# Kernel tuning notes

Measured on AMD Instinct MI355X. Metric: run time of the kernel, lower is better.

Reference implementation:

```python
import jax, jax.numpy as jnp
import numpy as np

N_EMBED = 768
NUM_EXPERTS = 8
TOP_K = 2
B, S = 2, 2048
THRESH = 1e-09


def setup_inputs() -> dict:
    key = jax.random.key(0)
    ks = jax.random.split(key, 12)
    d, e, f = N_EMBED, NUM_EXPERTS, 4 * N_EMBED
    s_in = 1.0 / np.sqrt(d)
    s_hid = 1.0 / np.sqrt(f)
    return {
        'x': jax.random.normal(ks[0], (B, S, d), jnp.float32),
        'noise': jax.random.normal(ks[1], (B * S, e), jnp.float32),
        'Wg': jax.random.normal(ks[2], (d, e), jnp.float32) * s_in,
        'bg': jnp.zeros((e,), jnp.float32),
        'Wn': jax.random.normal(ks[3], (d, e), jnp.float32) * s_in,
        'bn': jnp.zeros((e,), jnp.float32),
        'W1': jax.random.normal(ks[4], (e, d, f), jnp.float32) * s_in,
        'b1': jnp.zeros((e, f), jnp.float32),
        'W2': jax.random.normal(ks[5], (e, f, d), jnp.float32) * s_hid,
        'b2': jnp.zeros((e, d), jnp.float32),
    }


def reference(x, noise, Wg, bg, Wn, bn, W1, b1, W2, b2):
    Bsz, Ssz, d = x.shape
    T = Bsz * Ssz
    xr = x.reshape(T, d)  # [T, d]

    # Noisy top-k router
    logits = xr @ Wg + bg                     # [T, E]
    noise_logits = xr @ Wn + bn               # [T, E]
    noisy = logits + noise * jax.nn.softplus(noise_logits)
    vals, idx = jax.lax.top_k(noisy, TOP_K)   # [T, K]
    rows = jnp.arange(T)[:, None]
    sparse = jnp.full_like(noisy, -jnp.inf).at[rows, idx].set(vals)
    probs = jax.nn.softmax(sparse, axis=-1)   # [T, E]; zeros off top-k

    # Gate = prob masked by activation threshold (matches torch dispatch)
    gate = jnp.where(probs > THRESH, probs, 0.0)  # [T, E]

    # Dense per-expert MLP (dropout=0 -> identity), combined by gate
    h = jax.nn.relu(jnp.einsum('td,edf->etf', xr, W1) + b1[:, None, :])  # [E, T, 4d]
    y = jnp.einsum('etf,efd->etd', h, W2) + b2[:, None, :]               # [E, T, d]
    out = jnp.einsum('te,etd->td', gate, y)                              # [T, d]
    return out.reshape(Bsz, Ssz, d)
```

## Files before the change

kernel.cpp:

```cpp
#include <hip/hip_runtime.h>
#include <math.h>

typedef unsigned short u16;
typedef unsigned int u32;

#define D_EMB 768
#define F_HID 3072
#define N_TOK 4096
#define N_PAIR 8192
#define GATE_TH 1e-9f

typedef float f32x4 __attribute__((ext_vector_type(4)));
typedef __bf16 bfrag __attribute__((ext_vector_type(8)));

__device__ inline float b2f(u16 u) {
    union { float f; u32 i; } c; c.i = ((u32)u) << 16; return c.f;
}
__device__ inline u16 f2b(float f) {
    union { float f; u32 i; } c; c.f = f;
    u32 r = c.i + 0x7FFFu + ((c.i >> 16) & 1u);
    return (u16)(r >> 16);
}
__device__ inline f32x4 mfma16(bfrag a, bfrag b, f32x4 c) {
    return __builtin_amdgcn_mfma_f32_16x16x32_bf16(a, b, c, 0, 0, 0);
}
__device__ inline void gll16(const u16* g, u16* l) {
    __builtin_amdgcn_global_load_lds(
        (const __attribute__((address_space(1))) u32*)g,
        (__attribute__((address_space(3))) u32*)l, 16, 0, 0);
}
__device__ inline void sbar() {
    asm volatile("" ::: "memory");
    __builtin_amdgcn_s_barrier();
    asm volatile("" ::: "memory");
}
__device__ inline void waitv0() { asm volatile("s_waitcnt vmcnt(0)" ::: "memory"); }
__device__ inline void waitv4() { asm volatile("s_waitcnt vmcnt(4)" ::: "memory"); }

__global__ void moe_init_kernel(int* __restrict__ cnt) {
    if (threadIdx.x < 8) cnt[threadIdx.x] = 0;
}
__global__ __launch_bounds__(256) void moe_zero_kernel(uint4* __restrict__ out) {
    int i = blockIdx.x * 256 + threadIdx.x;
    out[i] = make_uint4(0, 0, 0, 0);
}

__global__ __launch_bounds__(64) void moe_router_v3(
    const float* __restrict__ x, const float* __restrict__ noise,
    const float* __restrict__ Wg, const float* __restrict__ bg,
    const float* __restrict__ Wn, const float* __restrict__ bn,
    int* __restrict__ tk_e, float* __restrict__ tk_g, int* __restrict__ cnt,
    ushort4* __restrict__ xb4)
{
    const int lane = threadIdx.x;
    const int tl = lane & 7, q = lane >> 3;
    const int t = blockIdx.x * 8 + tl;
    float ag[8] = {}, an[8] = {};
    const float4* xp = (const float4*)(x + (size_t)t * D_EMB + q * 96);
#pragma unroll 4
    for (int k4 = 0; k4 < 24; k4++) {
        float4 xv = xp[k4];
        const int kb = q * 96 + k4 * 4;
#pragma unroll
        for (int c = 0; c < 4; c++) {
            float xc = (&xv.x)[c];
            const float4* wg = (const float4*)(Wg + (size_t)(kb + c) * 8);
            const float4* wn = (const float4*)(Wn + (size_t)(kb + c) * 8);
            float4 g0 = wg[0], g1 = wg[1], n0 = wn[0], n1 = wn[1];
            ag[0] += xc * g0.x; ag[1] += xc * g0.y; ag[2] += xc * g0.z; ag[3] += xc * g0.w;
            ag[4] += xc * g1.x; ag[5] += xc * g1.y; ag[6] += xc * g1.z; ag[7] += xc * g1.w;
            an[0] += xc * n0.x; an[1] += xc * n0.y; an[2] += xc * n0.z; an[3] += xc * n0.w;
            an[4] += xc * n1.x; an[5] += xc * n1.y; an[6] += xc * n1.z; an[7] += xc * n1.w;
        }
    }
#pragma unroll
    for (int e = 0; e < 8; e++) {
        ag[e] += __shfl_xor(ag[e], 8);  an[e] += __shfl_xor(an[e], 8);
        ag[e] += __shfl_xor(ag[e], 16); an[e] += __shfl_xor(an[e], 16);
        ag[e] += __shfl_xor(ag[e], 32); an[e] += __shfl_xor(an[e], 32);
    }
    if (q == 0) {
        float best = -INFINITY, sec = -INFINITY; int be = 0, se = 0;
#pragma unroll
        for (int e = 0; e < 8; e++) {
            float nl = an[e] + bn[e];
            float sp = nl > 0.f ? nl + log1pf(expf(-nl)) : log1pf(expf(nl));
            float v = ag[e] + bg[e] + noise[(size_t)t * 8 + e] * sp;
            if (v > best) { sec = best; se = be; best = v; be = e; }
            else if (v > sec) { sec = v; se = e; }
        }
        float ex = expf(sec - best);
        float g1 = 1.f / (1.f + ex), g2 = ex / (1.f + ex);
        tk_e[t * 2 + 0] = (g1 > GATE_TH) ? be : -1; tk_g[t * 2 + 0] = g1;
        tk_e[t * 2 + 1] = (g2 > GATE_TH) ? se : -1; tk_g[t * 2 + 1] = g2;
        if (g1 > GATE_TH) atomicAdd(&cnt[be], 1);
        if (g2 > GATE_TH) atomicAdd(&cnt[se], 1);
    }
    if (xb4) {
        const int t0 = blockIdx.x * 8;
        for (int i = lane; i < 8 * 192; i += 64) {
            int ti = i / 192, c = i - ti * 192;
            float4 v = *(const float4*)(x + (size_t)(t0 + ti) * D_EMB + c * 4);
            ushort4 o;
            o.x = f2b(v.x); o.y = f2b(v.y); o.z = f2b(v.z); o.w = f2b(v.w);
            xb4[(size_t)(t0 + ti) * 192 + c] = o;
        }
    }
}

__global__ void moe_offsets_kernel(const int* __restrict__ cnt,
                                   int* __restrict__ off, int* __restrict__ cursor) {
    if (threadIdx.x == 0) {
        int s = 0;
        for (int e = 0; e < 8; e++) { off[e] = s; cursor[e] = s; s += cnt[e]; }
    }
}
__global__ void moe_scatter_kernel(const int* __restrict__ tk_e, const float* __restrict__ tk_g,
                                   int* __restrict__ cursor, int* __restrict__ plist,
                                   float* __restrict__ pg, int* __restrict__ pos) {
    int i = blockIdx.x * 256 + threadIdx.x;
    if (i < N_PAIR) {
        int e = tk_e[i];
        if (e >= 0) {
            int p = atomicAdd(&cursor[e], 1);
            plist[p] = i >> 1;
            pg[p] = tk_g[i];
            pos[i] = p;
        }
    }
}

__global__ __launch_bounds__(256) void moe_transcvt_kernel(
    const float* __restrict__ in, u16* __restrict__ out, int R, int C) {
    __shared__ float tile[32][33];
    const int z = blockIdx.z;
    const int c0 = blockIdx.x * 32, r0 = blockIdx.y * 32;
    const int tx = threadIdx.x & 31, ty = threadIdx.x >> 5;
    const size_t base = (size_t)z * R * C;
#pragma unroll
    for (int j = 0; j < 32; j += 8)
        tile[ty + j][tx] = in[base + (size_t)(r0 + ty + j) * C + c0 + tx];
    __syncthreads();
#pragma unroll
    for (int j = 0; j < 32; j += 8)
        out[base + (size_t)(c0 + ty + j) * R + r0 + tx] = f2b(tile[tx][ty + j]);
}

__global__ __launch_bounds__(256) void moe_ffn1_kernel(
    const u16* __restrict__ xb, const u16* __restrict__ wt, const float* __restrict__ b1,
    const int* __restrict__ plist, const int* __restrict__ cnt, const int* __restrict__ off,
    u16* __restrict__ h, int P0, int P1)
{
    __shared__ __align__(16) u16 As[2][128 * 32];
    __shared__ __align__(16) u16 Bs[2][128 * 32];
    const int GX = 24, GY = 16;
    int f = blockIdx.x + GX * (blockIdx.y + GY * blockIdx.z);
    int swz = (f & 7) * 384 + (f >> 3);
    int nb = swz % GX;
    int t2 = swz / GX;
    int mb = t2 % GY;
    int e  = t2 / GY;

    int lo = off[e], hi = lo + cnt[e];
    if (lo < P0) lo = P0;
    if (hi > P1) hi = P1;
    const int Cl = hi - lo;
    if (Cl <= 0) return;
    const int n0 = nb * 128;
    const int tid = threadIdx.x;
    const int lane = tid & 63, wave = tid >> 6;
    const int wr = wave >> 1, wc = wave & 1;
    const int qq = lane >> 4, r = lane & 15;
    const int sig = (r & 3) ^ ((r >> 2) & 3);
    const int sa = ((qq ^ sig) << 3);
    const int srow = tid >> 2;
    const int gq = (tid & 3) ^ ((tid >> 2) & 3) ^ ((tid >> 4) & 3);

    const u16* bsrc[2];
#pragma unroll
    for (int j = 0; j < 2; j++)
        bsrc[j] = wt + ((size_t)e * F_HID + n0 + j * 64 + srow) * D_EMB + gq * 8;

    for (int m0 = mb * 128; m0 < Cl; m0 += GY * 128) {
        const u16* asrc[2];
#pragma unroll
        for (int j = 0; j < 2; j++) {
            int mr = m0 + j * 64 + srow;
            if (mr > Cl - 1) mr = Cl - 1;
            asrc[j] = xb + (size_t)plist[lo + mr] * D_EMB + gq * 8;
        }
        f32x4 acc[4][4] = {};

        auto stage = [&](int kt, int buf) {
            const int k0 = kt * 32;
#pragma unroll
            for (int j = 0; j < 2; j++)
                gll16(asrc[j] + k0, &As[buf][j * 2048 + wave * 512]);
#pragma unroll
            for (int j = 0; j < 2; j++)
                gll16(bsrc[j] + k0, &Bs[buf][j * 2048 + wave * 512]);
        };
        auto compute = [&](int buf) {
            bfrag af[4], bf[4];
#pragma unroll
            for (int i = 0; i < 4; i++) {
                af[i] = *(const bfrag*)(&As[buf][(wr * 64 + i * 16 + r) * 32 + sa]);
                bf[i] = *(const bfrag*)(&Bs[buf][(wc * 64 + i * 16 + r) * 32 + sa]);
            }
#pragma unroll
            for (int mi = 0; mi < 4; mi++)
#pragma unroll
                for (int ni = 0; ni < 4; ni++)
                    acc[mi][ni] = mfma16(af[mi], bf[ni], acc[mi][ni]);
        };

        waitv0();
        stage(0, 0);
#pragma unroll 2
        for (int kt = 0; kt < 23; kt++) {
            stage(kt + 1, (kt + 1) & 1);
            waitv4(); sbar();
            compute(kt & 1);
            sbar();
        }
        waitv0(); sbar();
        compute(1);

#pragma unroll
        for (int mi = 0; mi < 4; mi++)
#pragma unroll
            for (int ni = 0; ni < 4; ni++) {
                int col = n0 + wc * 64 + ni * 16 + r;
                float bias = b1[(size_t)e * F_HID + col];
#pragma unroll
                for (int i = 0; i < 4; i++) {
                    int m = m0 + wr * 64 + mi * 16 + qq * 4 + i;
                    if (m < Cl) {
                        float v = acc[mi][ni][i] + bias;
                        h[(size_t)(lo - P0 + m) * F_HID + col] = f2b(v > 0.f ? v : 0.f);
                    }
                }
            }
        sbar();
    }
}

__global__ __launch_bounds__(256) void moe_ffn2_kernel(
    const u16* __restrict__ h, const u16* __restrict__ wt, const float* __restrict__ b2,
    const int* __restrict__ cnt, const int* __restrict__ off,
    float* __restrict__ y, int P0, int P1)
{
    __shared__ __align__(16) u16 As[2][128 * 32];
    __shared__ __align__(16) u16 Bs[2][128 * 32];
    const int GX = 6, GY = 16;
    int f = blockIdx.x + GX * (blockIdx.y + GY * blockIdx.z);
    int swz = (f & 7) * 96 + (f >> 3);
    int nb = swz % GX;
    int t2 = swz / GX;
    int mb = t2 % GY;
    int e  = t2 / GY;

    int lo = off[e], hi = lo + cnt[e];
    if (lo < P0) lo = P0;
    if (hi > P1) hi = P1;
    const int Cl = hi - lo;
    if (Cl <= 0) return;
    const int n0 = nb * 128;
    const int tid = threadIdx.x;
    const int lane = tid & 63, wave = tid >> 6;
    const int wr = wave >> 1, wc = wave & 1;
    const int qq = lane >> 4, r = lane & 15;
    const int sig = (r & 3) ^ ((r >> 2) & 3);
    const int sa = ((qq ^ sig) << 3);
    const int srow = tid >> 2;
    const int gq = (tid & 3) ^ ((tid >> 2) & 3) ^ ((tid >> 4) & 3);

    const u16* bsrc[2];
#pragma unroll
    for (int j = 0; j < 2; j++)
        bsrc[j] = wt + ((size_t)e * D_EMB + n0 + j * 64 + srow) * F_HID + gq * 8;

    for (int m0 = mb * 128; m0 < Cl; m0 += GY * 128) {
        const u16* asrc[2];
#pragma unroll
        for (int j = 0; j < 2; j++) {
            int mr = m0 + j * 64 + srow;
            if (mr > Cl - 1) mr = Cl - 1;
            asrc[j] = h + (size_t)(lo - P0 + mr) * F_HID + gq * 8;
        }
        f32x4 acc[4][4] = {};

        auto stage = [&](int kt, int buf) {
            const int k0 = kt * 32;
#pragma unroll
            for (int j = 0; j < 2; j++)
                gll16(asrc[j] + k0, &As[buf][j * 2048 + wave * 512]);
#pragma unroll
            for (int j = 0; j < 2; j++)
                gll16(bsrc[j] + k0, &Bs[buf][j * 2048 + wave * 512]);
        };
        auto compute = [&](int buf) {
            bfrag af[4], bf[4];
#pragma unroll
            for (int i = 0; i < 4; i++) {
                af[i] = *(const bfrag*)(&As[buf][(wr * 64 + i * 16 + r) * 32 + sa]);
                bf[i] = *(const bfrag*)(&Bs[buf][(wc * 64 + i * 16 + r) * 32 + sa]);
            }
#pragma unroll
            for (int mi = 0; mi < 4; mi++)
#pragma unroll
                for (int ni = 0; ni < 4; ni++)
                    acc[mi][ni] = mfma16(af[mi], bf[ni], acc[mi][ni]);
        };

        waitv0();
        stage(0, 0);
#pragma unroll 2
        for (int kt = 0; kt < 95; kt++) {
            stage(kt + 1, (kt + 1) & 1);
            waitv4(); sbar();
            compute(kt & 1);
            sbar();
        }
        waitv0(); sbar();
        compute(1);

#pragma unroll
        for (int mi = 0; mi < 4; mi++)
#pragma unroll
            for (int ni = 0; ni < 4; ni++) {
                int col = n0 + wc * 64 + ni * 16 + r;
                float bias = b2[(size_t)e * D_EMB + col];
#pragma unroll
                for (int i = 0; i < 4; i++) {
                    int m = m0 + wr * 64 + mi * 16 + qq * 4 + i;
                    if (m < Cl)
                        y[(size_t)(lo + m) * D_EMB + col] = acc[mi][ni][i] + bias;
                }
            }
        sbar();
    }
}

__global__ __launch_bounds__(256) void moe_combine_kernel(
    const float* __restrict__ y, const int* __restrict__ tk_e,
    const float* __restrict__ tk_g, const int* __restrict__ pos,
    float4* __restrict__ out)
{
    int i = blockIdx.x * 256 + threadIdx.x;
    int t = i / 192;
    int c = i - t * 192;
    float4 a = make_float4(0.f, 0.f, 0.f, 0.f);
#pragma unroll
    for (int k = 0; k < 2; k++) {
        int e = tk_e[t * 2 + k];
        if (e >= 0) {
            float g = tk_g[t * 2 + k];
            float4 v = ((const float4*)(y + (size_t)pos[t * 2 + k] * D_EMB))[c];
            a.x += g * v.x; a.y += g * v.y; a.z += g * v.z; a.w += g * v.w;
        }
    }
    out[i] = a;
}

#define XSTR 776
#define HSTR 3080
#define BMF 8
__global__ __launch_bounds__(256) void moe_ffn_fused_f32(
    const float* __restrict__ x,
    const float* __restrict__ w1, const float* __restrict__ b1,
    const float* __restrict__ w2, const float* __restrict__ b2,
    const int* __restrict__ plist, const float* __restrict__ pg,
    const int* __restrict__ cnt, const int* __restrict__ off,
    float* __restrict__ out)
{
    __shared__ __align__(16) u16 xs[BMF * XSTR];
    __shared__ __align__(16) u16 hs[BMF * HSTR];
    const int e = blockIdx.x;
    const int Cl = cnt[e];
    if (Cl <= 0) return;
    const int O = off[e];
    const int tid = threadIdx.x;
    for (int t0 = blockIdx.y * BMF; t0 < Cl; t0 += gridDim.y * BMF) {
        for (int ci = tid; ci < BMF * 192; ci += 256) {
            int row = ci / 192, c = ci - row * 192;
            float4 v = make_float4(0.f, 0.f, 0.f, 0.f);
            if (t0 + row < Cl) {
                int tok = plist[O + t0 + row];
                v = *(const float4*)(x + (size_t)tok * D_EMB + c * 4);
            }
            u16* d = &xs[row * XSTR + c * 4];
            d[0] = f2b(v.x); d[1] = f2b(v.y); d[2] = f2b(v.z); d[3] = f2b(v.w);
        }
        __syncthreads();
        for (int wi = tid; wi < BMF * 768; wi += 256) {
            int row = wi / 768, nc = wi - row * 768;
            int n0 = nc * 4;
            float a0 = 0, a1 = 0, a2 = 0, a3 = 0;
            const float* wp = w1 + (size_t)e * D_EMB * F_HID + n0;
            const u16* xr = &xs[row * XSTR];
            for (int k = 0; k < D_EMB; k++) {
                float4 wv = *(const float4*)(wp + (size_t)k * F_HID);
                float xv = b2f(xr[k]);
                a0 += xv * wv.x; a1 += xv * wv.y; a2 += xv * wv.z; a3 += xv * wv.w;
            }
            const float* bp = b1 + (size_t)e * F_HID + n0;
            u16* hp = &hs[row * HSTR + n0];
            float v;
            v = a0 + bp[0]; hp[0] = f2b(v > 0.f ? v : 0.f);
            v = a1 + bp[1]; hp[1] = f2b(v > 0.f ? v : 0.f);
            v = a2 + bp[2]; hp[2] = f2b(v > 0.f ? v : 0.f);
            v = a3 + bp[3]; hp[3] = f2b(v > 0.f ? v : 0.f);
        }
        __syncthreads();
        for (int wi = tid; wi < BMF * 192; wi += 256) {
            int row = wi / 192, nc = wi - row * 192;
            int n0 = nc * 4;
            float a0 = 0, a1 = 0, a2 = 0, a3 = 0;
            const float* wp = w2 + (size_t)e * F_HID * D_EMB + n0;
            const u16* hr = &hs[row * HSTR];
            for (int k = 0; k < F_HID; k++) {
                float4 wv = *(const float4*)(wp + (size_t)k * D_EMB);
                float hv = b2f(hr[k]);
                a0 += hv * wv.x; a1 += hv * wv.y; a2 += hv * wv.z; a3 += hv * wv.w;
            }
            if (t0 + row < Cl) {
                int p = O + t0 + row;
                int tok = plist[p];
                float g = pg[p];
                const float* bp = b2 + (size_t)e * D_EMB + n0;
                float* op = out + (size_t)tok * D_EMB + n0;
                atomicAdd(&op[0], g * (a0 + bp[0]));
                atomicAdd(&op[1], g * (a1 + bp[1]));
                atomicAdd(&op[2], g * (a2 + bp[2]));
                atomicAdd(&op[3], g * (a3 + bp[3]));
            }
        }
        __syncthreads();
    }
}

extern "C" void kernel_launch(void* const* d_in, const int* in_sizes, int n_in,
                              void* d_out, int out_size, void* d_ws, size_t ws_size,
                              hipStream_t stream) {
    const float* x     = (const float*)d_in[0];
    const float* noise = (const float*)d_in[1];
    const float* Wg    = (const float*)d_in[2];
    const float* bg    = (const float*)d_in[3];
    const float* Wn    = (const float*)d_in[4];
    const float* bn    = (const float*)d_in[5];
    const float* W1    = (const float*)d_in[6];
    const float* b1    = (const float*)d_in[7];
    const float* W2    = (const float*)d_in[8];
    const float* b2    = (const float*)d_in[9];
    float* out = (float*)d_out;

    char* ws = (char*)d_ws;
    int*   cnt    = (int*)(ws + 0);
    int*   off    = (int*)(ws + 256);
    int*   cursor = (int*)(ws + 512);
    int*   tk_e   = (int*)(ws + 1024);
    float* tk_g   = (float*)(ws + 33792);
    int*   plist  = (int*)(ws + 66560);
    float* pg     = (float*)(ws + 99328);
    int*   pos    = (int*)(ws + 132096);
    const size_t SMALL  = 164864;
    const size_t WSZ    = 37748736ull;
    const size_t XB_SZ  = 6291456ull;
    const size_t Y_SZ   = 25165824ull;
    const size_t H_FULL = 50331648ull;

    const size_t NEED_A = SMALL + WSZ + XB_SZ + Y_SZ + H_FULL;

    if (ws_size >= NEED_A) {
        u16*   wt = (u16*)(ws + SMALL);
        u16*   xb = (u16*)(ws + SMALL + WSZ);
        float* y  = (float*)(ws + SMALL + WSZ + XB_SZ);
        u16*   h  = (u16*)(ws + SMALL + WSZ + XB_SZ + Y_SZ);

        moe_init_kernel<<<dim3(1), dim3(64), 0, stream>>>(cnt);
        moe_router_v3<<<dim3(512), dim3(64), 0, stream>>>(
            x, noise, Wg, bg, Wn, bn, tk_e, tk_g, cnt, (ushort4*)xb);
        moe_offsets_kernel<<<dim3(1), dim3(64), 0, stream>>>(cnt, off, cursor);
        moe_scatter_kernel<<<dim3(N_PAIR / 256), dim3(256), 0, stream>>>(
            tk_e, tk_g, cursor, plist, pg, pos);
        moe_transcvt_kernel<<<dim3(F_HID / 32, D_EMB / 32, 8), dim3(256), 0, stream>>>(
            W1, wt, D_EMB, F_HID);
        moe_ffn1_kernel<<<dim3(24, 16, 8), dim3(256), 0, stream>>>(
            xb, wt, b1, plist, cnt, off, h, 0, N_PAIR);
        moe_transcvt_kernel<<<dim3(D_EMB / 32, F_HID / 32, 8), dim3(256), 0, stream>>>(
            W2, wt, F_HID, D_EMB);
        moe_ffn2_kernel<<<dim3(6, 16, 8), dim3(256), 0, stream>>>(
            h, wt, b2, cnt, off, y, 0, N_PAIR);
        moe_combine_kernel<<<dim3(3072), dim3(256), 0, stream>>>(
            y, tk_e, tk_g, pos, (float4*)out);
        (void)in_sizes; (void)n_in; (void)out_size;
        return;
    }

    const size_t B_BASE = SMALL + 2 * WSZ + XB_SZ + Y_SZ;
    int pchunk = 0;
    for (int p = N_PAIR; p >= 512; p >>= 1) {
        if (B_BASE + (size_t)p * F_HID * 2 <= ws_size) { pchunk = p; break; }
    }

    moe_init_kernel<<<dim3(1), dim3(64), 0, stream>>>(cnt);
    moe_router_v3<<<dim3(512), dim3(64), 0, stream>>>(
        x, noise, Wg, bg, Wn, bn, tk_e, tk_g, cnt,
        pchunk > 0 ? (ushort4*)(ws + SMALL + 2 * WSZ) : (ushort4*)0);
    moe_offsets_kernel<<<dim3(1), dim3(64), 0, stream>>>(cnt, off, cursor);
    moe_scatter_kernel<<<dim3(N_PAIR / 256), dim3(256), 0, stream>>>(
        tk_e, tk_g, cursor, plist, pg, pos);

    if (pchunk > 0) {
        u16*   w1t = (u16*)(ws + SMALL);
        u16*   w2t = (u16*)(ws + SMALL + WSZ);
        u16*   xb  = (u16*)(ws + SMALL + 2 * WSZ);
        float* y   = (float*)(ws + SMALL + 2 * WSZ + XB_SZ);
        u16*   h   = (u16*)(ws + B_BASE);
        moe_transcvt_kernel<<<dim3(F_HID / 32, D_EMB / 32, 8), dim3(256), 0, stream>>>(
            W1, w1t, D_EMB, F_HID);
        moe_transcvt_kernel<<<dim3(D_EMB / 32, F_HID / 32, 8), dim3(256), 0, stream>>>(
            W2, w2t, F_HID, D_EMB);
        for (int c = 0; c < N_PAIR / pchunk; c++) {
            int P0 = c * pchunk, P1 = P0 + pchunk;
            moe_ffn1_kernel<<<dim3(24, 16, 8), dim3(256), 0, stream>>>(
                xb, w1t, b1, plist, cnt, off, h, P0, P1);
            moe_ffn2_kernel<<<dim3(6, 16, 8), dim3(256), 0, stream>>>(
                h, w2t, b2, cnt, off, y, P0, P1);
        }
        moe_combine_kernel<<<dim3(3072), dim3(256), 0, stream>>>(
            y, tk_e, tk_g, pos, (float4*)out);
    } else {
        moe_zero_kernel<<<dim3(3072), dim3(256), 0, stream>>>((uint4*)out);
        moe_ffn_fused_f32<<<dim3(8, 192), dim3(256), 0, stream>>>(
            x, W1, b1, W2, b2, plist, pg, cnt, off, out);
    }
    (void)in_sizes; (void)n_in; (void)out_size;
}
```

Baseline: 512.0 us.

## Vectorize weight transpose-convert and simplify LDS swizzle in expert GEMMs

The fp32-to-bf16 weight transpose now processes 128x32 tiles, reading each row with float4 loads and writing 16-byte packed bf16 rows, which cuts the number of narrow global accesses. Both FFN GEMM kernels switch to a simpler XOR swizzle for the LDS layout, use scalar source pointers instead of small pointer arrays, and drop the unroll-2 pragma on the k-loop. ffn2 also clamps A-row indices to the chunk capacity. The new swizzle has to stay consistent between the global_load_lds write pattern and the fragment reads, and its bank-conflict behaviour changes.

```diff
diff --git a/kernel.cpp b/kernel.cpp
--- a/kernel.cpp
+++ b/kernel.cpp
@@ -12,6 +12,7 @@
 
 typedef float f32x4 __attribute__((ext_vector_type(4)));
 typedef __bf16 bfrag __attribute__((ext_vector_type(8)));
+typedef u16 u16x8 __attribute__((ext_vector_type(8)));
 
 __device__ inline float b2f(u16 u) {
     union { float f; u32 i; } c; c.i = ((u32)u) << 16; return c.f;
@@ -132,18 +133,34 @@
 
 __global__ __launch_bounds__(256) void moe_transcvt_kernel(
     const float* __restrict__ in, u16* __restrict__ out, int R, int C) {
-    __shared__ float tile[32][33];
+    __shared__ float tile[128][33];
     const int z = blockIdx.z;
-    const int c0 = blockIdx.x * 32, r0 = blockIdx.y * 32;
-    const int tx = threadIdx.x & 31, ty = threadIdx.x >> 5;
+    const int c0 = blockIdx.x * 32, r0 = blockIdx.y * 128;
     const size_t base = (size_t)z * R * C;
-#pragma unroll
-    for (int j = 0; j < 32; j += 8)
-        tile[ty + j][tx] = in[base + (size_t)(r0 + ty + j) * C + c0 + tx];
+    const int t = threadIdx.x;
+    {
+        const int row = t >> 1, cb = (t & 1) * 16;
+        const float* src = in + base + (size_t)(r0 + row) * C + c0 + cb;
+        float4 v0 = *(const float4*)(src + 0);
+        float4 v1 = *(const float4*)(src + 4);
+        float4 v2 = *(const float4*)(src + 8);
+        float4 v3 = *(const float4*)(src + 12);
+        float* d = &tile[row][cb];
+        d[0]  = v0.x; d[1]  = v0.y; d[2]  = v0.z; d[3]  = v0.w;
+        d[4]  = v1.x; d[5]  = v1.y; d[6]  = v1.z; d[7]  = v1.w;
+        d[8]  = v2.x; d[9]  = v2.y; d[10] = v2.z; d[11] = v2.w;
+        d[12] = v3.x; d[13] = v3.y; d[14] = v3.z; d[15] = v3.w;
+    }
     __syncthreads();
-#pragma unroll
-    for (int j = 0; j < 32; j += 8)
-        out[base + (size_t)(c0 + ty + j) * R + r0 + tx] = f2b(tile[tx][ty + j]);
+    const int c = t >> 3, ua = t & 7;
+#pragma unroll
+    for (int k = 0; k < 2; k++) {
+        int rr = (ua + k * 8) * 8;
+        u16x8 o;
+#pragma unroll
+        for (int i = 0; i < 8; i++) o[i] = f2b(tile[rr + i][c]);
+        *(u16x8*)(out + base + (size_t)(c0 + c) * R + r0 + rr) = o;
+    }
 }
 
 __global__ __launch_bounds__(256) void moe_ffn1_kernel(
@@ -171,41 +188,33 @@
     const int lane = tid & 63, wave = tid >> 6;
     const int wr = wave >> 1, wc = wave & 1;
     const int qq = lane >> 4, r = lane & 15;
-    const int sig = (r & 3) ^ ((r >> 2) & 3);
-    const int sa = ((qq ^ sig) << 3);
+    const int qa = (qq ^ ((r >> 1) & 3)) * 8;
     const int srow = tid >> 2;
-    const int gq = (tid & 3) ^ ((tid >> 2) & 3) ^ ((tid >> 4) & 3);
-
-    const u16* bsrc[2];
-#pragma unroll
-    for (int j = 0; j < 2; j++)
-        bsrc[j] = wt + ((size_t)e * F_HID + n0 + j * 64 + srow) * D_EMB + gq * 8;
+    const int gq = (tid & 3) ^ ((tid >> 3) & 3);
+
+    const u16* bsrc0 = wt + ((size_t)e * F_HID + n0 + srow) * D_EMB + gq * 8;
+    const u16* bsrc1 = bsrc0 + (size_t)64 * D_EMB;
 
     for (int m0 = mb * 128; m0 < Cl; m0 += GY * 128) {
-        const u16* asrc[2];
-#pragma unroll
-        for (int j = 0; j < 2; j++) {
-            int mr = m0 + j * 64 + srow;
-            if (mr > Cl - 1) mr = Cl - 1;
-            asrc[j] = xb + (size_t)plist[lo + mr] * D_EMB + gq * 8;
-        }
+        int mr0 = m0 + srow;      if (mr0 > Cl - 1) mr0 = Cl - 1;
+        int mr1 = m0 + 64 + srow; if (mr1 > Cl - 1) mr1 = Cl - 1;
+        const u16* asrc0 = xb + (size_t)plist[lo + mr0] * D_EMB + gq * 8;
+        const u16* asrc1 = xb + (size_t)plist[lo + mr1] * D_EMB + gq * 8;
         f32x4 acc[4][4] = {};
 
         auto stage = [&](int kt, int buf) {
             const int k0 = kt * 32;
-#pragma unroll
-            for (int j = 0; j < 2; j++)
-                gll16(asrc[j] + k0, &As[buf][j * 2048 + wave * 512]);
-#pragma unroll
-            for (int j = 0; j < 2; j++)
-                gll16(bsrc[j] + k0, &Bs[buf][j * 2048 + wave * 512]);
+            gll16(asrc0 + k0, &As[buf][wave * 512]);
+            gll16(asrc1 + k0, &As[buf][2048 + wave * 512]);
+            gll16(bsrc0 + k0, &Bs[buf][wave * 512]);
+            gll16(bsrc1 + k0, &Bs[buf][2048 + wave * 512]);
         };
         auto compute = [&](int buf) {
             bfrag af[4], bf[4];
 #pragma unroll
             for (int i = 0; i < 4; i++) {
-                af[i] = *(const bfrag*)(&As[buf][(wr * 64 + i * 16 + r) * 32 + sa]);
-                bf[i] = *(const bfrag*)(&Bs[buf][(wc * 64 + i * 16 + r) * 32 + sa]);
+                af[i] = *(const bfrag*)(&As[buf][(wr * 64 + i * 16 + r) * 32 + qa]);
+                bf[i] = *(const bfrag*)(&Bs[buf][(wc * 64 + i * 16 + r) * 32 + qa]);
             }
 #pragma unroll
             for (int mi = 0; mi < 4; mi++)
@@ -216,7 +225,6 @@
 
         waitv0();
         stage(0, 0);
-#pragma unroll 2
         for (int kt = 0; kt < 23; kt++) {
             stage(kt + 1, (kt + 1) & 1);
             waitv4(); sbar();
@@ -270,41 +278,36 @@
     const int lane = tid & 63, wave = tid >> 6;
     const int wr = wave >> 1, wc = wave & 1;
     const int qq = lane >> 4, r = lane & 15;
-    const int sig = (r & 3) ^ ((r >> 2) & 3);
-    const int sa = ((qq ^ sig) << 3);
+    const int qa = (qq ^ ((r >> 1) & 3)) * 8;
     const int srow = tid >> 2;
-    const int gq = (tid & 3) ^ ((tid >> 2) & 3) ^ ((tid >> 4) & 3);
-
-    const u16* bsrc[2];
-#pragma unroll
-    for (int j = 0; j < 2; j++)
-        bsrc[j] = wt + ((size_t)e * D_EMB + n0 + j * 64 + srow) * F_HID + gq * 8;
+    const int gq = (tid & 3) ^ ((tid >> 3) & 3);
+    const int hcap = P1 - P0;
+
+    const u16* bsrc0 = wt + ((size_t)e * D_EMB + n0 + srow) * F_HID + gq * 8;
+    const u16* bsrc1 = bsrc0 + (size_t)64 * F_HID;
 
     for (int m0 = mb * 128; m0 < Cl; m0 += GY * 128) {
-        const u16* asrc[2];
-#pragma unroll
-        for (int j = 0; j < 2; j++) {
-            int mr = m0 + j * 64 + srow;
-            if (mr > Cl - 1) mr = Cl - 1;
-            asrc[j] = h + (size_t)(lo - P0 + mr) * F_HID + gq * 8;
-        }
+        int mr0 = m0 + srow;      if (mr0 > Cl - 1) mr0 = Cl - 1;
+        int mr1 = m0 + 64 + srow; if (mr1 > Cl - 1) mr1 = Cl - 1;
+        if (mr0 >= hcap) mr0 = hcap - 1;
+        if (mr1 >= hcap) mr1 = hcap - 1;
+        const u16* asrc0 = h + (size_t)(lo - P0 + mr0) * F_HID + gq * 8;
+        const u16* asrc1 = h + (size_t)(lo - P0 + mr1) * F_HID + gq * 8;
         f32x4 acc[4][4] = {};
 
         auto stage = [&](int kt, int buf) {
             const int k0 = kt * 32;
-#pragma unroll
-            for (int j = 0; j < 2; j++)
-                gll16(asrc[j] + k0, &As[buf][j * 2048 + wave * 512]);
-#pragma unroll
-            for (int j = 0; j < 2; j++)
-                gll16(bsrc[j] + k0, &Bs[buf][j * 2048 + wave * 512]);
+            gll16(asrc0 + k0, &As[buf][wave * 512]);
+            gll16(asrc1 + k0, &As[buf][2048 + wave * 512]);
+            gll16(bsrc0 + k0, &Bs[buf][wave * 512]);
+            gll16(bsrc1 + k0, &Bs[buf][2048 + wave * 512]);
         };
         auto compute = [&](int buf) {
             bfrag af[4], bf[4];
 #pragma unroll
             for (int i = 0; i < 4; i++) {
-                af[i] = *(const bfrag*)(&As[buf][(wr * 64 + i * 16 + r) * 32 + sa]);
-                bf[i] = *(const bfrag*)(&Bs[buf][(wc * 64 + i * 16 + r) * 32 + sa]);
+                af[i] = *(const bfrag*)(&As[buf][(wr * 64 + i * 16 + r) * 32 + qa]);
+                bf[i] = *(const bfrag*)(&Bs[buf][(wc * 64 + i * 16 + r) * 32 + qa]);
             }
 #pragma unroll
             for (int mi = 0; mi < 4; mi++)
@@ -315,7 +318,6 @@
 
         waitv0();
         stage(0, 0);
-#pragma unroll 2
         for (int kt = 0; kt < 95; kt++) {
             stage(kt + 1, (kt + 1) & 1);
             waitv4(); sbar();
@@ -484,11 +486,11 @@
         moe_offsets_kernel<<<dim3(1), dim3(64), 0, stream>>>(cnt, off, cursor);
         moe_scatter_kernel<<<dim3(N_PAIR / 256), dim3(256), 0, stream>>>(
             tk_e, tk_g, cursor, plist, pg, pos);
-        moe_transcvt_kernel<<<dim3(F_HID / 32, D_EMB / 32, 8), dim3(256), 0, stream>>>(
+        moe_transcvt_kernel<<<dim3(F_HID / 32, D_EMB / 128, 8), dim3(256), 0, stream>>>(
             W1, wt, D_EMB, F_HID);
         moe_ffn1_kernel<<<dim3(24, 16, 8), dim3(256), 0, stream>>>(
             xb, wt, b1, plist, cnt, off, h, 0, N_PAIR);
-        moe_transcvt_kernel<<<dim3(D_EMB / 32, F_HID / 32, 8), dim3(256), 0, stream>>>(
+        moe_transcvt_kernel<<<dim3(D_EMB / 32, F_HID / 128, 8), dim3(256), 0, stream>>>(
             W2, wt, F_HID, D_EMB);
         moe_ffn2_kernel<<<dim3(6, 16, 8), dim3(256), 0, stream>>>(
             h, wt, b2, cnt, off, y, 0, N_PAIR);
@@ -518,9 +520,9 @@
         u16*   xb  = (u16*)(ws + SMALL + 2 * WSZ);
         float* y   = (float*)(ws + SMALL + 2 * WSZ + XB_SZ);
         u16*   h   = (u16*)(ws + B_BASE);
-        moe_transcvt_kernel<<<dim3(F_HID / 32, D_EMB / 32, 8), dim3(256), 0, stream>>>(
+        moe_transcvt_kernel<<<dim3(F_HID / 32, D_EMB / 128, 8), dim3(256), 0, stream>>>(
             W1, w1t, D_EMB, F_HID);
-        moe_transcvt_kernel<<<dim3(D_EMB / 32, F_HID / 32, 8), dim3(256), 0, stream>>>(
+        moe_transcvt_kernel<<<dim3(D_EMB / 32, F_HID / 128, 8), dim3(256), 0, stream>>>(
             W2, w2t, F_HID, D_EMB);
         for (int c = 0; c < N_PAIR / pchunk; c++) {
             int P0 = c * pchunk, P1 = P0 + pchunk;
```

Measured after the change: 469.8 us. -8.2%, faster.
